# Kernel optimization log

Measured on AMD Instinct MI355X. Metric: run time of the kernel, lower is better.

The kernel has to match this reference:

```python
import jax, jax.numpy as jnp
import numpy as np

B_, P_, C_, S_ = 32, 16384, 2, 256   # batch, n_points, n_classes, box_size
LAT, ENC, H, NL = 10, 10, 64, 4       # latent dim, pos_enc_dim, hidden, n_layers


def setup_inputs() -> dict:
    key = jax.random.key(0)
    ks = jax.random.split(key, 10)
    z = jax.random.normal(ks[0], (B_, LAT), jnp.float32)
    orientation = jax.random.normal(ks[1], (B_, 3, 3), jnp.float32)  # rotation matrices
    shift = jax.random.normal(ks[2], (B_, 2), jnp.float32)           # pixel shifts
    # Gaussian center positions in box units [-0.37, 0.37] (stay inside box)
    model_positions = (jax.random.uniform(ks[3], (P_, 3), jnp.float32) - 0.5) * 0.74
    D_in = 6 * ENC + LAT
    W_in = jax.random.normal(ks[4], (D_in, H), jnp.float32) / jnp.sqrt(D_in * 1.0)
    W_layers = jax.random.normal(ks[5], (NL, H, H), jnp.float32) / jnp.sqrt(H * 1.0)
    W_out1 = jax.random.normal(ks[6], (H, 3), jnp.float32) / jnp.sqrt(H * 1.0)
    # original zero-fills this; use small values so the displacement path is nontrivial
    W_out2 = jax.random.normal(ks[7], (3, 3), jnp.float32) * 0.01
    amp = 30.0 * jnp.ones((C_, P_), jnp.float32)
    ampvar = 0.5 * jax.random.normal(ks[8], (C_, P_), jnp.float32)
    A = jnp.ones((C_,), jnp.float32)                 # smoother amplitudes
    Bp = jnp.linspace(0.01, 0.05, C_, dtype=jnp.float32)  # smoother widths
    return dict(z=z, orientation=orientation, shift=shift,
                model_positions=model_positions, W_in=W_in, W_layers=W_layers,
                W_out1=W_out1, W_out2=W_out2, amp=amp, ampvar=ampvar, A=A, Bp=Bp)


def positional_encoding(pos, enc_dim, box_size):
    # geometric frequency ladder from 1 to box_size/2, sin/cos per coordinate -> 6*enc_dim feats
    freqs = (box_size / 2.0) ** (jnp.arange(enc_dim, dtype=pos.dtype) / (enc_dim - 1))
    k = 2.0 * jnp.pi * pos[..., None] * freqs        # [..., 3, enc_dim]
    enc = jnp.concatenate([jnp.sin(k), jnp.cos(k)], axis=-1)
    return enc.reshape(pos.shape[:-1] + (6 * enc_dim,))


def mlp(x, W_in, W_layers, W1, W2):
    h = x @ W_in                                     # input layer, no activation
    for i in range(W_layers.shape[0]):
        h = jax.nn.elu(h @ W_layers[i])              # LinearBlock = Linear + ELU
    return jax.nn.elu(h @ W1) @ W2                   # output head


def points_to_images(pos2d, amps, S):
    # pos2d [B,P,2] in box units; amps [B,C,P]; bilinear splat -> [B,C,S,S]
    px = jnp.clip((pos2d + 0.5) * S, 0.0, S - 1.001)
    x0 = jnp.floor(px[..., 0]).astype(jnp.int32)
    y0 = jnp.floor(px[..., 1]).astype(jnp.int32)
    fx = px[..., 0] - x0
    fy = px[..., 1] - y0
    x1 = jnp.minimum(x0 + 1, S - 1)
    y1 = jnp.minimum(y0 + 1, S - 1)
    idx = jnp.stack([y0 * S + x0, y0 * S + x1, y1 * S + x0, y1 * S + x1], 0)      # [4,B,P]
    w = jnp.stack([(1 - fx) * (1 - fy), fx * (1 - fy), (1 - fx) * fy, fx * fy], 0)  # [4,B,P]

    def splat_one(idx_b, w_b, amp_b):
        # idx_b [4,P], w_b [4,P], amp_b [C,P]
        C = amp_b.shape[0]
        vals = amp_b[:, None, :] * w_b[None]          # [C,4,P]
        img = jnp.zeros((C, S * S), vals.dtype)
        img = img.at[:, idx_b.reshape(-1)].add(vals.reshape(C, -1))
        return img.reshape(C, S, S)

    return jax.vmap(splat_one, in_axes=(1, 1, 0))(idx, w, amps)


def fourier_smooth(ims, A, Bcoef):
    # ims [B,C,S,S] -> per-class Gaussian filter in Fourier space, sum over classes
    S = ims.shape[-1]
    c = (jnp.arange(S) - S // 2).astype(ims.dtype)
    R = jnp.sqrt(c[:, None] ** 2 + c[None, :] ** 2)   # centered radial grid
    FF = jnp.exp(-(Bcoef[:, None, None] ** 2) * R) * A[:, None, None] ** 2  # [C,S,S]
    FF = jnp.fft.ifftshift(FF, axes=(-2, -1))
    out = jnp.fft.ifft2(jnp.sum(FF[None] * jnp.fft.fft2(ims), axis=1))
    return jnp.real(out)                              # [B,S,S]


def fourier_shift_2d(ims, sx, sy):
    S = ims.shape[-1]
    f = jnp.fft.fftfreq(S).astype(ims.dtype)
    phase = jnp.exp(-2j * jnp.pi * (f[None, None, :] * sx[:, None, None]
                                    + f[None, :, None] * sy[:, None, None]))
    return jnp.real(jnp.fft.ifft2(jnp.fft.fft2(ims) * phase))


def reference(z, orientation, shift, model_positions, W_in, W_layers, W_out1, W_out2, amp, ampvar, A, Bp):
    B = z.shape[0]
    P = model_positions.shape[0]
    enc = positional_encoding(model_positions, ENC, S_)            # [P, 6*ENC]
    x = jnp.concatenate([
        jnp.broadcast_to(enc[None], (B, P, enc.shape[-1])),
        jnp.broadcast_to(z[:, None, :], (B, P, z.shape[-1]))], axis=-1)
    displacements = mlp(x, W_in, W_layers, W_out1, W_out2)         # [B,P,3]
    final_positions = model_positions[None] + displacements        # [B,P,3]
    projected = jnp.einsum('bij,bpj->bpi', orientation, final_positions)[..., :2]
    wamp = amp * jax.nn.softmax(ampvar, axis=0)                    # [C,P]
    wamp = jnp.broadcast_to(wamp[None], (B,) + wamp.shape)
    imgs = points_to_images(projected, wamp, S_)                   # [B,C,S,S]
    imgs = fourier_smooth(imgs, A, Bp)                             # [B,S,S]
    imgs = fourier_shift_2d(imgs, shift[:, 0], shift[:, 1])
    return imgs, final_positions, displacements
```

## Files before the change

### kernel.cpp

```cpp
#include <hip/hip_runtime.h>
#include <math.h>

static constexpr int Bn = 32, Pn = 16384, Cn = 2, Sn = 256;
static constexpr int KXD = 132;

#define TWO_PI_F 6.28318530717958647692f
#define SPLAT_SCALE 2048.0f
#define SPLAT_INV   (1.0f / 2048.0f)

typedef float v4f __attribute__((ext_vector_type(4)));
typedef short v8s __attribute__((ext_vector_type(8)));

__device__ __forceinline__ float elu_f(float x) {
  return x > 0.0f ? x : (__expf(x) - 1.0f);
}

__device__ __forceinline__ unsigned short f2bf(float x) {
  unsigned int u = __float_as_uint(x);
  u = u + 0x7FFFu + ((u >> 16) & 1u);
  return (unsigned short)(u >> 16);
}

__device__ __forceinline__ int cvt_pk_bf16(float lo, float hi) {
  int r;
  asm("v_cvt_pk_bf16_f32 %0, %1, %2" : "=v"(r) : "v"(lo), "v"(hi));
  return r;
}

__device__ __forceinline__ void fft256(float* re, float* im,
                                       const float* twr, const float* twi,
                                       int lane, bool inverse) {
  #pragma unroll
  for (int q = 0; q < 4; q++) {
    int t = lane + q * 64;
    int r = (int)(__brev((unsigned)t) >> 24);
    if (t < r) {
      float a = re[t]; re[t] = re[r]; re[r] = a;
      float b = im[t]; im[t] = im[r]; im[r] = b;
    }
  }
  __syncthreads();
  #pragma unroll
  for (int s = 1; s <= 8; s++) {
    int half = 1 << (s - 1);
    #pragma unroll
    for (int q = 0; q < 2; q++) {
      int bf = lane + q * 64;
      int j = bf & (half - 1);
      int grp = bf >> (s - 1);
      int i0 = (grp << s) + j;
      int i1 = i0 + half;
      int tx = j << (8 - s);
      float wr = twr[tx];
      float wi = twi[tx];
      if (inverse) wi = -wi;
      float xr = re[i1], xi = im[i1];
      float tr = fmaf(xr, wr, -xi * wi);
      float ti = fmaf(xr, wi,  xi * wr);
      float ar = re[i0], ai = im[i0];
      re[i0] = ar + tr; im[i0] = ai + ti;
      re[i1] = ar - tr; im[i1] = ai - ti;
    }
    __syncthreads();
  }
}

__global__ __launch_bounds__(64) void enc_kernel(const float* __restrict__ mp,
                                                 const float* __restrict__ W_in,
                                                 float* __restrict__ encpart) {
  __shared__ float ebuf[60][64];
  int tid = threadIdx.x;
  int p = blockIdx.x * 64 + tid;
  #pragma unroll
  for (int c = 0; c < 3; c++) {
    float pos = mp[p * 3 + c];
    #pragma unroll
    for (int i = 0; i < 10; i++) {
      float freq = powf(128.0f, (float)i / 9.0f);
      float ang = (TWO_PI_F * pos) * freq;
      ebuf[c * 20 + i][tid]      = sinf(ang);
      ebuf[c * 20 + 10 + i][tid] = cosf(ang);
    }
  }
  float h[64];
  #pragma unroll
  for (int j = 0; j < 64; j++) h[j] = 0.0f;
  for (int k = 0; k < 60; k++) {
    float ek = ebuf[k][tid];
    const float* wr = W_in + k * 64;
    #pragma unroll
    for (int j = 0; j < 64; j++) h[j] = fmaf(ek, wr[j], h[j]);
  }
  float* o = encpart + (size_t)p * 64;
  #pragma unroll
  for (int j = 0; j < 64; j++) o[j] = h[j];
}

__global__ __launch_bounds__(256) void prep_kernel(const float* __restrict__ z,
                                                   const float* __restrict__ W_in,
                                                   const float* __restrict__ W_layers,
                                                   float* __restrict__ zpart,
                                                   unsigned short* __restrict__ Wfrag) {
  int idx = blockIdx.x * 256 + threadIdx.x;
  if (idx < 2048) {
    int b = idx >> 6, j = idx & 63;
    float s = 0.0f;
    #pragma unroll
    for (int k = 0; k < 10; k++) s = fmaf(z[b * 10 + k], W_in[(60 + k) * 64 + j], s);
    zpart[b * 64 + j] = s;
  } else {
    int t2 = idx - 2048;
    int L = t2 >> 9, m = (t2 >> 7) & 3, s = (t2 >> 6) & 1, lane = t2 & 63;
    #pragma unroll
    for (int i = 0; i < 8; i++) {
      int k = s * 32 + ((lane >> 4) * 8) + i;
      int j = m * 16 + (lane & 15);
      Wfrag[(size_t)t2 * 8 + i] = f2bf(W_layers[L * 4096 + k * 64 + j]);
    }
  }
}

__device__ __forceinline__ void regroup(const v4f* acc, v8s* Bf,
                                        int srcA, int srcB, bool hi) {
  union U4 { int u[4]; v8s v; };
  int pk[4][2];
  #pragma unroll
  for (int m = 0; m < 4; m++) {
    pk[m][0] = cvt_pk_bf16(acc[m][0], acc[m][1]);
    pk[m][1] = cvt_pk_bf16(acc[m][2], acc[m][3]);
  }
  #pragma unroll
  for (int s = 0; s < 2; s++) {
    int t00 = __builtin_amdgcn_ds_bpermute(srcA, pk[2 * s][0]);
    int t01 = __builtin_amdgcn_ds_bpermute(srcA, pk[2 * s + 1][0]);
    int t10 = __builtin_amdgcn_ds_bpermute(srcA, pk[2 * s][1]);
    int t11 = __builtin_amdgcn_ds_bpermute(srcA, pk[2 * s + 1][1]);
    int t20 = __builtin_amdgcn_ds_bpermute(srcB, pk[2 * s][0]);
    int t21 = __builtin_amdgcn_ds_bpermute(srcB, pk[2 * s + 1][0]);
    int t30 = __builtin_amdgcn_ds_bpermute(srcB, pk[2 * s][1]);
    int t31 = __builtin_amdgcn_ds_bpermute(srcB, pk[2 * s + 1][1]);
    U4 u;
    u.u[0] = hi ? t01 : t00;
    u.u[1] = hi ? t11 : t10;
    u.u[2] = hi ? t21 : t20;
    u.u[3] = hi ? t31 : t30;
    Bf[s] = u.v;
  }
}

__global__ __launch_bounds__(256) void mlp_mfma32_kernel(
    const float* __restrict__ encpart, const float* __restrict__ zpart,
    const unsigned short* __restrict__ Wfrag,
    const float* __restrict__ W_out1, const float* __restrict__ W_out2,
    const float* __restrict__ mp, const float* __restrict__ orient,
    const float* __restrict__ amp, const float* __restrict__ ampvar,
    float4* __restrict__ rec, int* __restrict__ stripCntSeg,
    float* __restrict__ out_fp, float* __restrict__ out_disp) {
  __shared__ int h16[16];
  int tid = threadIdx.x;
  int lane = tid & 63;
  int wave = tid >> 6;
  int wid = blockIdx.x * 4 + wave;
  int b = __builtin_amdgcn_readfirstlane(wid >> 9);
  int pbase = (wid & 511) * 32;
  int g = lane >> 4;
  int p0 = pbase + (lane & 15);
  int p1 = p0 + 16;

  if (tid < 16) h16[tid] = 0;
  __syncthreads();

  union U4 { int u[4]; v8s v; };

  v8s Bf0[2], Bf1[2];
  #pragma unroll
  for (int s = 0; s < 2; s++) {
    int k0 = s * 32 + g * 8;
    const float4* z4 = (const float4*)(zpart + b * 64 + k0);
    float4 z0 = z4[0], z1 = z4[1];
    {
      const float4* e4 = (const float4*)(encpart + (size_t)p0 * 64 + k0);
      float4 e0 = e4[0], e1 = e4[1];
      U4 u;
      u.u[0] = cvt_pk_bf16(e0.x + z0.x, e0.y + z0.y);
      u.u[1] = cvt_pk_bf16(e0.z + z0.z, e0.w + z0.w);
      u.u[2] = cvt_pk_bf16(e1.x + z1.x, e1.y + z1.y);
      u.u[3] = cvt_pk_bf16(e1.z + z1.z, e1.w + z1.w);
      Bf0[s] = u.v;
    }
    {
      const float4* e4 = (const float4*)(encpart + (size_t)p1 * 64 + k0);
      float4 e0 = e4[0], e1 = e4[1];
      U4 u;
      u.u[0] = cvt_pk_bf16(e0.x + z0.x, e0.y + z0.y);
      u.u[1] = cvt_pk_bf16(e0.z + z0.z, e0.w + z0.w);
      u.u[2] = cvt_pk_bf16(e1.x + z1.x, e1.y + z1.y);
      u.u[3] = cvt_pk_bf16(e1.z + z1.z, e1.w + z1.w);
      Bf1[s] = u.v;
    }
  }

  int srcA = ((((lane >> 4) & 1) * 32) + (lane & 15)) << 2;
  int srcB = srcA + 64;
  bool hi = (lane >> 5) & 1;

  const v8s* WfragV = (const v8s*)Wfrag;
  v4f acc0[4], acc1[4];

  #pragma unroll 1
  for (int L = 0; L < 4; L++) {
    v8s Af[4][2];
    #pragma unroll
    for (int m = 0; m < 4; m++)
      #pragma unroll
      for (int s = 0; s < 2; s++)
        Af[m][s] = WfragV[(size_t)(((L * 4 + m) * 2 + s) * 64) + lane];

    #pragma unroll
    for (int m = 0; m < 4; m++) {
      acc0[m] = (v4f){0.f, 0.f, 0.f, 0.f};
      acc1[m] = (v4f){0.f, 0.f, 0.f, 0.f};
    }
    #pragma unroll
    for (int s = 0; s < 2; s++) {
      #pragma unroll
      for (int m = 0; m < 4; m++)
        acc0[m] = __builtin_amdgcn_mfma_f32_16x16x32_bf16(Af[m][s], Bf0[s], acc0[m], 0, 0, 0);
      #pragma unroll
      for (int m = 0; m < 4; m++)
        acc1[m] = __builtin_amdgcn_mfma_f32_16x16x32_bf16(Af[m][s], Bf1[s], acc1[m], 0, 0, 0);
    }

    #pragma unroll
    for (int m = 0; m < 4; m++)
      #pragma unroll
      for (int r = 0; r < 4; r++) {
        acc0[m][r] = elu_f(acc0[m][r]);
        acc1[m][r] = elu_f(acc1[m][r]);
      }

    if (L < 3) {
      regroup(acc0, Bf0, srcA, srcB, hi);
      regroup(acc1, Bf1, srcA, srcB, hi);
    }
  }

  float o00 = 0.f, o01 = 0.f, o02 = 0.f;
  float o10 = 0.f, o11 = 0.f, o12 = 0.f;
  #pragma unroll
  for (int m = 0; m < 4; m++) {
    int jb = m * 16 + g * 4;
    const float4* w4 = (const float4*)(W_out1 + jb * 3);
    float4 wa = w4[0], wb = w4[1], wc = w4[2];
    o00 += acc0[m][0] * wa.x + acc0[m][1] * wa.w + acc0[m][2] * wb.z + acc0[m][3] * wc.y;
    o01 += acc0[m][0] * wa.y + acc0[m][1] * wb.x + acc0[m][2] * wb.w + acc0[m][3] * wc.z;
    o02 += acc0[m][0] * wa.z + acc0[m][1] * wb.y + acc0[m][2] * wc.x + acc0[m][3] * wc.w;
    o10 += acc1[m][0] * wa.x + acc1[m][1] * wa.w + acc1[m][2] * wb.z + acc1[m][3] * wc.y;
    o11 += acc1[m][0] * wa.y + acc1[m][1] * wb.x + acc1[m][2] * wb.w + acc1[m][3] * wc.z;
    o12 += acc1[m][0] * wa.z + acc1[m][1] * wb.y + acc1[m][2] * wc.x + acc1[m][3] * wc.w;
  }
  o00 += __shfl_xor(o00, 16, 64); o00 += __shfl_xor(o00, 32, 64);
  o01 += __shfl_xor(o01, 16, 64); o01 += __shfl_xor(o01, 32, 64);
  o02 += __shfl_xor(o02, 16, 64); o02 += __shfl_xor(o02, 32, 64);
  o10 += __shfl_xor(o10, 16, 64); o10 += __shfl_xor(o10, 32, 64);
  o11 += __shfl_xor(o11, 16, 64); o11 += __shfl_xor(o11, 32, 64);
  o12 += __shfl_xor(o12, 16, 64); o12 += __shfl_xor(o12, 32, 64);

  o00 = elu_f(o00); o01 = elu_f(o01); o02 = elu_f(o02);
  o10 = elu_f(o10); o11 = elu_f(o11); o12 = elu_f(o12);

  float W0 = W_out2[0], W1 = W_out2[1], W2 = W_out2[2];
  float W3 = W_out2[3], W4 = W_out2[4], W5 = W_out2[5];
  float W6 = W_out2[6], W7 = W_out2[7], W8 = W_out2[8];

  float d00 = o00 * W0 + o01 * W3 + o02 * W6;
  float d01 = o00 * W1 + o01 * W4 + o02 * W7;
  float d02 = o00 * W2 + o01 * W5 + o02 * W8;
  float d10 = o10 * W0 + o11 * W3 + o12 * W6;
  float d11 = o10 * W1 + o11 * W4 + o12 * W7;
  float d12 = o10 * W2 + o11 * W5 + o12 * W8;

  float m00 = mp[p0 * 3 + 0], m01 = mp[p0 * 3 + 1], m02 = mp[p0 * 3 + 2];
  float m10 = mp[p1 * 3 + 0], m11 = mp[p1 * 3 + 1], m12 = mp[p1 * 3 + 2];
  float f00 = m00 + d00, f01 = m01 + d01, f02 = m02 + d02;
  float f10 = m10 + d10, f11 = m11 + d11, f12 = m12 + d12;

  size_t ob0 = ((size_t)b * Pn + p0) * 3;
  size_t ob1 = ((size_t)b * Pn + p1) * 3;
  if (g == 2) {
    out_disp[ob0 + 0] = d00; out_disp[ob0 + 1] = d01; out_disp[ob0 + 2] = d02;
    out_fp[ob0 + 0] = f00; out_fp[ob0 + 1] = f01; out_fp[ob0 + 2] = f02;
  }
  if (g == 3) {
    out_disp[ob1 + 0] = d10; out_disp[ob1 + 1] = d11; out_disp[ob1 + 2] = d12;
    out_fp[ob1 + 0] = f10; out_fp[ob1 + 1] = f11; out_fp[ob1 + 2] = f12;
  }

  const float* R = orient + b * 9;
  float px0 = R[0] * f00 + R[1] * f01 + R[2] * f02;
  float py0 = R[3] * f00 + R[4] * f01 + R[5] * f02;
  float px1 = R[0] * f10 + R[1] * f11 + R[2] * f12;
  float py1 = R[3] * f10 + R[4] * f11 + R[5] * f12;

  float a00 = ampvar[p0], a01 = ampvar[Pn + p0];
  float mx0 = fmaxf(a00, a01);
  float e00 = __expf(a00 - mx0), e01 = __expf(a01 - mx0);
  float inv0 = 1.0f / (e00 + e01);
  float w00a = amp[p0] * e00 * inv0;
  float w01a = amp[Pn + p0] * e01 * inv0;
  float a10 = ampvar[p1], a11 = ampvar[Pn + p1];
  float mx1 = fmaxf(a10, a11);
  float e10 = __expf(a10 - mx1), e11 = __expf(a11 - mx1);
  float inv1 = 1.0f / (e10 + e11);
  float w10a = amp[p1] * e10 * inv1;
  float w11a = amp[Pn + p1] * e11 * inv1;

  float pxp0 = fminf(fmaxf((px0 + 0.5f) * 256.0f, 0.0f), 254.999f);
  float pyp0 = fminf(fmaxf((py0 + 0.5f) * 256.0f, 0.0f), 254.999f);
  float pxp1 = fminf(fmaxf((px1 + 0.5f) * 256.0f, 0.0f), 254.999f);
  float pyp1 = fminf(fmaxf((py1 + 0.5f) * 256.0f, 0.0f), 254.999f);

  if (g == 0) {
    atomicAdd(&h16[((int)pyp0) >> 4], 1);
    rec[(size_t)b * Pn + p0] = make_float4(pxp0, pyp0, w00a, w01a);
  }
  if (g == 1) {
    atomicAdd(&h16[((int)pyp1) >> 4], 1);
    rec[(size_t)b * Pn + p1] = make_float4(pxp1, pyp1, w10a, w11a);
  }
  __syncthreads();
  int bblk = __builtin_amdgcn_readfirstlane(blockIdx.x >> 7);
  int seg  = __builtin_amdgcn_readfirstlane((blockIdx.x & 127) >> 4);
  if (tid < 16 && h16[tid] != 0)
    atomicAdd(&stripCntSeg[(bblk * 8 + seg) * 16 + tid], h16[tid]);
}

__global__ __launch_bounds__(256) void scatter16_kernel(const float4* __restrict__ rec,
                                                        const int* __restrict__ stripCntSeg,
                                                        float4* __restrict__ sorted) {
  __shared__ int tot[16], start[16], cur[16];
  int blk = blockIdx.x;
  int b = blk >> 3, seg = blk & 7;
  int tid = threadIdx.x;
  int myoff = 0;
  if (tid < 16) {
    int acc = 0, so = 0;
    #pragma unroll
    for (int s = 0; s < 8; s++) {
      int c = stripCntSeg[(b * 8 + s) * 16 + tid];
      if (s < seg) so += c;
      acc += c;
    }
    tot[tid] = acc; myoff = so;
  }
  __syncthreads();
  if (tid == 0) { int a = 0; for (int i = 0; i < 16; i++) { start[i] = a; a += tot[i]; } }
  __syncthreads();
  if (tid < 16) cur[tid] = start[tid] + myoff;
  __syncthreads();
  int base = seg * 2048;
  for (int i = base + tid; i < base + 2048; i += 256) {
    float4 r = rec[(size_t)b * Pn + i];
    int strip = ((int)r.y) >> 4;
    int slot = atomicAdd(&cur[strip], 1);
    sorted[(size_t)b * Pn + slot] = r;
  }
}

__global__ __launch_bounds__(256) void splat_fft_rows_T(const float4* __restrict__ sorted,
                                                        const int* __restrict__ stripCntSeg,
                                                        float2* __restrict__ ws1) {
  __shared__ float sre[16][257], sim[16][257];
  __shared__ float twr[128], twi[128];
  __shared__ int tot[16], start[16];
  int tid = threadIdx.x;
  int lane = tid & 63, wave = tid >> 6;
  int blk = blockIdx.x;
  int chunk = blk & 15, b = blk >> 4;
  for (int t = tid; t < 128; t += 256) {
    float ang = -TWO_PI_F * (float)t / 256.0f;
    twr[t] = cosf(ang); twi[t] = sinf(ang);
  }
  if (tid < 16) {
    int acc = 0;
    #pragma unroll
    for (int s = 0; s < 8; s++) acc += stripCntSeg[(b * 8 + s) * 16 + tid];
    tot[tid] = acc;
  }
  float* fre = &sre[0][0];
  float* fim = &sim[0][0];
  int* ire = (int*)fre;
  int* iim = (int*)fim;
  for (int j = tid; j < 16 * 257; j += 256) { ire[j] = 0; iim[j] = 0; }
  __syncthreads();
  if (tid == 0) { int a = 0; for (int i = 0; i < 16; i++) { start[i] = a; a += tot[i]; } }
  __syncthreads();

  int lo = (chunk > 0) ? start[chunk - 1] : start[0];
  int hi = start[chunk] + tot[chunk];
  int ybase = chunk * 16;
  const float4* rb = sorted + (size_t)b * Pn;
  for (int i = lo + tid; i < hi; i += 256) {
    float4 r = rb[i];
    int y0 = (int)r.y;
    int d = y0 - ybase;
    if (d >= -1 && d <= 15) {
      int x0 = (int)r.x;
      int x1 = x0 + 1;
      float fx = r.x - (float)x0, fy = r.y - (float)y0;
      float w00 = (1.f - fx) * (1.f - fy), w10 = fx * (1.f - fy);
      float w01 = (1.f - fx) * fy,         w11 = fx * fy;
      if (d >= 0) {
        int o = d * 257;
        atomicAdd(&ire[o + x0], __float2int_rn(r.z * w00 * SPLAT_SCALE));
        atomicAdd(&ire[o + x1], __float2int_rn(r.z * w10 * SPLAT_SCALE));
        atomicAdd(&iim[o + x0], __float2int_rn(r.w * w00 * SPLAT_SCALE));
        atomicAdd(&iim[o + x1], __float2int_rn(r.w * w10 * SPLAT_SCALE));
      }
      if (d <= 14) {
        int o = (d + 1) * 257;
        atomicAdd(&ire[o + x0], __float2int_rn(r.z * w01 * SPLAT_SCALE));
        atomicAdd(&ire[o + x1], __float2int_rn(r.z * w11 * SPLAT_SCALE));
        atomicAdd(&iim[o + x0], __float2int_rn(r.w * w01 * SPLAT_SCALE));
        atomicAdd(&iim[o + x1], __float2int_rn(r.w * w11 * SPLAT_SCALE));
      }
    }
  }
  __syncthreads();
  for (int j = tid; j < 16 * 257; j += 256) {
    fre[j] = (float)ire[j] * SPLAT_INV;
    fim[j] = (float)iim[j] * SPLAT_INV;
  }
  __syncthreads();

  #pragma unroll 1
  for (int rnd = 0; rnd < 4; rnd++) {
    int row = wave * 4 + rnd;
    fft256(&sre[row][0], &sim[row][0], twr, twi, lane, false);
  }
  #pragma unroll 1
  for (int ko = 0; ko < 9; ko++) {
    int kx = ko * 16 + (tid >> 4);
    int ysub = tid & 15;
    if (kx < KXD) {
      int m = (256 - kx) & 255;
      float zr = sre[ysub][kx], zi = sim[ysub][kx];
      float mr = sre[ysub][m],  mi = sim[ysub][m];
      float z0r = 0.5f * (zr + mr), z0i = 0.5f * (zi - mi);
      float z1r = 0.5f * (zi + mi), z1i = 0.5f * (mr - zr);
      size_t y = (size_t)(chunk * 16 + ysub);
      ws1[((size_t)(b * 2 + 0) * KXD + kx) * 256 + y] = make_float2(z0r, z0i);
      ws1[((size_t)(b * 2 + 1) * KXD + kx) * 256 + y] = make_float2(z1r, z1i);
    }
  }
}

__global__ __launch_bounds__(256) void fft_mid_T(const float2* __restrict__ ws1,
                                                 float2* __restrict__ A2,
                                                 const float* __restrict__ shift,
                                                 const float* __restrict__ Aarr,
                                                 const float* __restrict__ Bparr) {
  __shared__ float sre[4][257], sim[4][257];
  __shared__ float wre[4][257], wim[4][257];
  __shared__ float twr[128], twi[128];
  int tid = threadIdx.x;
  int lane = tid & 63, wave = tid >> 6;
  int blk = blockIdx.x;
  int b = blk / 33, c33 = blk % 33;
  int kx = c33 * 4 + wave;
  for (int t = tid; t < 128; t += 256) {
    float ang = -TWO_PI_F * (float)t / 256.0f;
    twr[t] = cosf(ang); twi[t] = sinf(ang);
  }
  __syncthreads();
  float A0 = Aarr[0], A1 = Aarr[1], B0 = Bparr[0], B1 = Bparr[1];
  float sy = shift[b * 2 + 1];
  const float2* r0 = ws1 + ((size_t)(b * 2 + 0) * KXD + kx) * 256;
  const float2* r1 = ws1 + ((size_t)(b * 2 + 1) * KXD + kx) * 256;
  #pragma unroll
  for (int q = 0; q < 4; q++) {
    int i = lane + q * 64;
    float2 v0 = r0[i], v1 = r1[i];
    sre[wave][i] = v0.x; sim[wave][i] = v0.y;
    wre[wave][i] = v1.x; wim[wave][i] = v1.y;
  }
  fft256(&sre[wave][0], &sim[wave][0], twr, twi, lane, false);
  fft256(&wre[wave][0], &wim[wave][0], twr, twi, lane, false);
  float rx = (kx <= 128) ? (float)kx : (float)(256 - kx);
  #pragma unroll
  for (int q = 0; q < 4; q++) {
    int ky = lane + q * 64;
    float ry = (ky <= 128) ? (float)ky : (float)(256 - ky);
    float R = sqrtf(rx * rx + ry * ry);
    float FF0 = A0 * A0 * __expf(-B0 * B0 * R);
    float FF1 = A1 * A1 * __expf(-B1 * B1 * R);
    float Gr = FF0 * sre[wave][ky] + FF1 * wre[wave][ky];
    float Gi = FF0 * sim[wave][ky] + FF1 * wim[wave][ky];
    float fk = (float)((ky < 128) ? ky : ky - 256) / 256.0f;
    float th = -TWO_PI_F * fk * sy;
    float cc = __cosf(th), ss = __sinf(th);
    sre[wave][ky] = Gr * cc - Gi * ss;
    sim[wave][ky] = Gr * ss + Gi * cc;
  }
  fft256(&sre[wave][0], &sim[wave][0], twr, twi, lane, true);
  const float inv = 1.0f / 256.0f;
  int kx0 = c33 * 4;
  #pragma unroll 1
  for (int yo = 0; yo < 4; yo++) {
    int ksub = tid & 3;
    int y = yo * 64 + (tid >> 2);
    int kxw = kx0 + ksub;
    float vr = sre[ksub][y] * inv, vi = sim[ksub][y] * inv;
    if (kxw <= 128)
      A2[(size_t)b * 65536 + (size_t)y * 256 + kxw] = make_float2(vr, vi);
    if (kxw >= 1 && kxw <= 127)
      A2[(size_t)b * 65536 + (size_t)y * 256 + (256 - kxw)] = make_float2(vr, -vi);
  }
}

__global__ __launch_bounds__(256) void fft_final_pk(const float2* __restrict__ A2t,
                                                    const float* __restrict__ shift,
                                                    float* __restrict__ out_imgs) {
  __shared__ float re[4][257], im[4][257];
  __shared__ float twr[128], twi[128];
  int tid = threadIdx.x;
  int lane = tid & 63, wave = tid >> 6;
  int blk = blockIdx.x;
  int b = blk >> 5, grp = blk & 31;
  int y0 = grp * 8 + wave * 2;
  int y1 = y0 + 1;
  for (int t = tid; t < 128; t += 256) {
    float ang = -TWO_PI_F * (float)t / 256.0f;
    twr[t] = cosf(ang); twi[t] = sinf(ang);
  }
  float sx = shift[b * 2 + 0];
  const float2* row0 = A2t + (size_t)b * 65536 + (size_t)y0 * 256;
  const float2* row1 = A2t + (size_t)b * 65536 + (size_t)y1 * 256;
  float g0r[4], g0i[4], g1r[4], g1i[4];
  #pragma unroll
  for (int q = 0; q < 4; q++) {
    int k = lane + q * 64;
    float2 v0 = row0[k], v1 = row1[k];
    float fk = (float)((k < 128) ? k : k - 256) / 256.0f;
    float th = -TWO_PI_F * fk * sx;
    float c = __cosf(th), s = __sinf(th);
    g0r[q] = v0.x * c - v0.y * s;  g0i[q] = v0.x * s + v0.y * c;
    g1r[q] = v1.x * c - v1.y * s;  g1i[q] = v1.x * s + v1.y * c;
  }
  int src = (64 - lane) & 63;
  float s0r[4], s0i[4], s1r[4], s1i[4];
  #pragma unroll
  for (int j = 0; j < 4; j++) {
    s0r[j] = __shfl(g0r[j], src, 64);  s0i[j] = __shfl(g0i[j], src, 64);
    s1r[j] = __shfl(g1r[j], src, 64);  s1i[j] = __shfl(g1i[j], src, 64);
  }
  bool l0 = (lane == 0);
  #pragma unroll
  for (int q = 0; q < 4; q++) {
    const int qa = 3 - q;
    const int qb = (4 - q) & 3;
    float m0r = l0 ? s0r[qb] : s0r[qa];
    float m0i = l0 ? s0i[qb] : s0i[qa];
    float m1r = l0 ? s1r[qb] : s1r[qa];
    float m1i = l0 ? s1i[qb] : s1i[qa];
    float h0r = 0.5f * (g0r[q] + m0r), h0i = 0.5f * (g0i[q] - m0i);
    float h1r = 0.5f * (g1r[q] + m1r), h1i = 0.5f * (g1i[q] - m1i);
    int k = lane + q * 64;
    re[wave][k] = h0r - h1i;
    im[wave][k] = h0i + h1r;
  }
  fft256(&re[wave][0], &im[wave][0], twr, twi, lane, true);
  const float inv = 1.0f / 256.0f;
  float* o0 = out_imgs + (size_t)b * 65536 + (size_t)y0 * 256;
  float* o1 = out_imgs + (size_t)b * 65536 + (size_t)y1 * 256;
  #pragma unroll
  for (int q = 0; q < 4; q++) {
    int x = lane + q * 64;
    o0[x] = re[wave][x] * inv;
    o1[x] = im[wave][x] * inv;
  }
}

extern "C" void kernel_launch(void* const* d_in, const int* in_sizes, int n_in,
                              void* d_out, int out_size, void* d_ws, size_t ws_size,
                              hipStream_t stream) {
  (void)in_sizes; (void)n_in; (void)out_size; (void)ws_size;
  const float* z       = (const float*)d_in[0];
  const float* orient  = (const float*)d_in[1];
  const float* shift   = (const float*)d_in[2];
  const float* mp      = (const float*)d_in[3];
  const float* W_in    = (const float*)d_in[4];
  const float* W_layers= (const float*)d_in[5];
  const float* W_out1  = (const float*)d_in[6];
  const float* W_out2  = (const float*)d_in[7];
  const float* amp     = (const float*)d_in[8];
  const float* ampvar  = (const float*)d_in[9];
  const float* Aarr    = (const float*)d_in[10];
  const float* Bparr   = (const float*)d_in[11];

  char* ws0 = (char*)d_ws;
  float*  encpart = (float*)ws0;
  float2* A2      = (float2*)ws0;
  char* wsB = ws0 + 19922944;
  float2* ws1     = (float2*)wsB;
  float4* rec     = (float4*)(wsB + 17301504);
  float4* sorted  = (float4*)(wsB + 25690112);
  float*  zpart   = (float*)(wsB + 34078720);
  unsigned short* Wfrag = (unsigned short*)(wsB + 34078720 + 8192);
  int* stripCntSeg = (int*)(wsB + 34078720 + 40960);

  float* out      = (float*)d_out;
  float* out_imgs = out;
  float* out_fp   = out + (size_t)Bn * Sn * Sn;
  float* out_disp = out_fp + (size_t)Bn * Pn * 3;

  hipMemsetAsync(stripCntSeg, 0, Bn * 8 * 16 * sizeof(int), stream);
  enc_kernel<<<Pn / 64, 64, 0, stream>>>(mp, W_in, encpart);
  prep_kernel<<<16, 256, 0, stream>>>(z, W_in, W_layers, zpart, Wfrag);
  mlp_mfma32_kernel<<<(Bn * Pn / 32) / 4, 256, 0, stream>>>(
      encpart, zpart, Wfrag, W_out1, W_out2, mp, orient, amp, ampvar,
      rec, stripCntSeg, out_fp, out_disp);
  scatter16_kernel<<<Bn * 8, 256, 0, stream>>>(rec, stripCntSeg, sorted);
  splat_fft_rows_T<<<Bn * 16, 256, 0, stream>>>(sorted, stripCntSeg, ws1);
  fft_mid_T<<<Bn * 33, 256, 0, stream>>>(ws1, A2, shift, Aarr, Bparr);
  fft_final_pk<<<Bn * 32, 256, 0, stream>>>(A2, shift, out_imgs);
}
```

Before: 187.2 us.

## Process 64 points per wave in MLP kernel and fold counter memset into prep

Each wave now handles four 16-point column tiles instead of two. The per-layer weight fragments are reused across twice as many MFMAs, and every lane does useful epilogue work instead of only a quarter of them. The separate memset launch is replaced by zeroing the strip counters inside prep_kernel, which drops one stream operation. The cost is a doubled accumulator and B-fragment register footprint, which may lower occupancy, and half as many blocks in the grid.

```diff
diff --git a/kernel.cpp b/kernel.cpp
--- a/kernel.cpp
+++ b/kernel.cpp
@@ -100,8 +100,10 @@
                                                    const float* __restrict__ W_in,
                                                    const float* __restrict__ W_layers,
                                                    float* __restrict__ zpart,
-                                                   unsigned short* __restrict__ Wfrag) {
+                                                   unsigned short* __restrict__ Wfrag,
+                                                   int* __restrict__ stripCntSeg) {
   int idx = blockIdx.x * 256 + threadIdx.x;
+  stripCntSeg[idx] = 0;
   if (idx < 2048) {
     int b = idx >> 6, j = idx & 63;
     float s = 0.0f;
@@ -148,7 +150,7 @@
   }
 }
 
-__global__ __launch_bounds__(256) void mlp_mfma32_kernel(
+__global__ __launch_bounds__(256) void mlp_mfma64_kernel(
     const float* __restrict__ encpart, const float* __restrict__ zpart,
     const unsigned short* __restrict__ Wfrag,
     const float* __restrict__ W_out1, const float* __restrict__ W_out2,
@@ -161,51 +163,42 @@
   int lane = tid & 63;
   int wave = tid >> 6;
   int wid = blockIdx.x * 4 + wave;
-  int b = __builtin_amdgcn_readfirstlane(wid >> 9);
-  int pbase = (wid & 511) * 32;
+  int b = __builtin_amdgcn_readfirstlane(wid >> 8);
+  int pbase = (wid & 255) * 64;
   int g = lane >> 4;
-  int p0 = pbase + (lane & 15);
-  int p1 = p0 + 16;
+  int l15 = lane & 15;
 
   if (tid < 16) h16[tid] = 0;
   __syncthreads();
 
   union U4 { int u[4]; v8s v; };
 
-  v8s Bf0[2], Bf1[2];
+  v8s Bf[4][2];
   #pragma unroll
   for (int s = 0; s < 2; s++) {
     int k0 = s * 32 + g * 8;
     const float4* z4 = (const float4*)(zpart + b * 64 + k0);
     float4 z0 = z4[0], z1 = z4[1];
-    {
-      const float4* e4 = (const float4*)(encpart + (size_t)p0 * 64 + k0);
+    #pragma unroll
+    for (int k2 = 0; k2 < 4; k2++) {
+      int pk = pbase + k2 * 16 + l15;
+      const float4* e4 = (const float4*)(encpart + (size_t)pk * 64 + k0);
       float4 e0 = e4[0], e1 = e4[1];
       U4 u;
       u.u[0] = cvt_pk_bf16(e0.x + z0.x, e0.y + z0.y);
       u.u[1] = cvt_pk_bf16(e0.z + z0.z, e0.w + z0.w);
       u.u[2] = cvt_pk_bf16(e1.x + z1.x, e1.y + z1.y);
       u.u[3] = cvt_pk_bf16(e1.z + z1.z, e1.w + z1.w);
-      Bf0[s] = u.v;
-    }
-    {
-      const float4* e4 = (const float4*)(encpart + (size_t)p1 * 64 + k0);
-      float4 e0 = e4[0], e1 = e4[1];
-      U4 u;
-      u.u[0] = cvt_pk_bf16(e0.x + z0.x, e0.y + z0.y);
-      u.u[1] = cvt_pk_bf16(e0.z + z0.z, e0.w + z0.w);
-      u.u[2] = cvt_pk_bf16(e1.x + z1.x, e1.y + z1.y);
-      u.u[3] = cvt_pk_bf16(e1.z + z1.z, e1.w + z1.w);
-      Bf1[s] = u.v;
-    }
-  }
-
-  int srcA = ((((lane >> 4) & 1) * 32) + (lane & 15)) << 2;
+      Bf[k2][s] = u.v;
+    }
+  }
+
+  int srcA = ((((lane >> 4) & 1) * 32) + l15) << 2;
   int srcB = srcA + 64;
   bool hi = (lane >> 5) & 1;
 
   const v8s* WfragV = (const v8s*)Wfrag;
-  v4f acc0[4], acc1[4];
+  v4f acc[4][4];
 
   #pragma unroll 1
   for (int L = 0; L < 4; L++) {
@@ -217,120 +210,93 @@
         Af[m][s] = WfragV[(size_t)(((L * 4 + m) * 2 + s) * 64) + lane];
 
     #pragma unroll
-    for (int m = 0; m < 4; m++) {
-      acc0[m] = (v4f){0.f, 0.f, 0.f, 0.f};
-      acc1[m] = (v4f){0.f, 0.f, 0.f, 0.f};
-    }
-    #pragma unroll
-    for (int s = 0; s < 2; s++) {
+    for (int k2 = 0; k2 < 4; k2++)
       #pragma unroll
       for (int m = 0; m < 4; m++)
-        acc0[m] = __builtin_amdgcn_mfma_f32_16x16x32_bf16(Af[m][s], Bf0[s], acc0[m], 0, 0, 0);
+        acc[k2][m] = (v4f){0.f, 0.f, 0.f, 0.f};
+    #pragma unroll
+    for (int s = 0; s < 2; s++)
+      #pragma unroll
+      for (int k2 = 0; k2 < 4; k2++)
+        #pragma unroll
+        for (int m = 0; m < 4; m++)
+          acc[k2][m] = __builtin_amdgcn_mfma_f32_16x16x32_bf16(Af[m][s], Bf[k2][s], acc[k2][m], 0, 0, 0);
+
+    #pragma unroll
+    for (int k2 = 0; k2 < 4; k2++)
       #pragma unroll
       for (int m = 0; m < 4; m++)
-        acc1[m] = __builtin_amdgcn_mfma_f32_16x16x32_bf16(Af[m][s], Bf1[s], acc1[m], 0, 0, 0);
-    }
-
-    #pragma unroll
-    for (int m = 0; m < 4; m++)
+        #pragma unroll
+        for (int r = 0; r < 4; r++)
+          acc[k2][m][r] = elu_f(acc[k2][m][r]);
+
+    if (L < 3) {
       #pragma unroll
-      for (int r = 0; r < 4; r++) {
-        acc0[m][r] = elu_f(acc0[m][r]);
-        acc1[m][r] = elu_f(acc1[m][r]);
-      }
-
-    if (L < 3) {
-      regroup(acc0, Bf0, srcA, srcB, hi);
-      regroup(acc1, Bf1, srcA, srcB, hi);
-    }
-  }
-
-  float o00 = 0.f, o01 = 0.f, o02 = 0.f;
-  float o10 = 0.f, o11 = 0.f, o12 = 0.f;
+      for (int k2 = 0; k2 < 4; k2++)
+        regroup(acc[k2], Bf[k2], srcA, srcB, hi);
+    }
+  }
+
+  float o[4][3];
+  #pragma unroll
+  for (int k2 = 0; k2 < 4; k2++) { o[k2][0] = 0.f; o[k2][1] = 0.f; o[k2][2] = 0.f; }
   #pragma unroll
   for (int m = 0; m < 4; m++) {
     int jb = m * 16 + g * 4;
     const float4* w4 = (const float4*)(W_out1 + jb * 3);
     float4 wa = w4[0], wb = w4[1], wc = w4[2];
-    o00 += acc0[m][0] * wa.x + acc0[m][1] * wa.w + acc0[m][2] * wb.z + acc0[m][3] * wc.y;
-    o01 += acc0[m][0] * wa.y + acc0[m][1] * wb.x + acc0[m][2] * wb.w + acc0[m][3] * wc.z;
-    o02 += acc0[m][0] * wa.z + acc0[m][1] * wb.y + acc0[m][2] * wc.x + acc0[m][3] * wc.w;
-    o10 += acc1[m][0] * wa.x + acc1[m][1] * wa.w + acc1[m][2] * wb.z + acc1[m][3] * wc.y;
-    o11 += acc1[m][0] * wa.y + acc1[m][1] * wb.x + acc1[m][2] * wb.w + acc1[m][3] * wc.z;
-    o12 += acc1[m][0] * wa.z + acc1[m][1] * wb.y + acc1[m][2] * wc.x + acc1[m][3] * wc.w;
-  }
-  o00 += __shfl_xor(o00, 16, 64); o00 += __shfl_xor(o00, 32, 64);
-  o01 += __shfl_xor(o01, 16, 64); o01 += __shfl_xor(o01, 32, 64);
-  o02 += __shfl_xor(o02, 16, 64); o02 += __shfl_xor(o02, 32, 64);
-  o10 += __shfl_xor(o10, 16, 64); o10 += __shfl_xor(o10, 32, 64);
-  o11 += __shfl_xor(o11, 16, 64); o11 += __shfl_xor(o11, 32, 64);
-  o12 += __shfl_xor(o12, 16, 64); o12 += __shfl_xor(o12, 32, 64);
-
-  o00 = elu_f(o00); o01 = elu_f(o01); o02 = elu_f(o02);
-  o10 = elu_f(o10); o11 = elu_f(o11); o12 = elu_f(o12);
-
-  float W0 = W_out2[0], W1 = W_out2[1], W2 = W_out2[2];
-  float W3 = W_out2[3], W4 = W_out2[4], W5 = W_out2[5];
-  float W6 = W_out2[6], W7 = W_out2[7], W8 = W_out2[8];
-
-  float d00 = o00 * W0 + o01 * W3 + o02 * W6;
-  float d01 = o00 * W1 + o01 * W4 + o02 * W7;
-  float d02 = o00 * W2 + o01 * W5 + o02 * W8;
-  float d10 = o10 * W0 + o11 * W3 + o12 * W6;
-  float d11 = o10 * W1 + o11 * W4 + o12 * W7;
-  float d12 = o10 * W2 + o11 * W5 + o12 * W8;
-
-  float m00 = mp[p0 * 3 + 0], m01 = mp[p0 * 3 + 1], m02 = mp[p0 * 3 + 2];
-  float m10 = mp[p1 * 3 + 0], m11 = mp[p1 * 3 + 1], m12 = mp[p1 * 3 + 2];
-  float f00 = m00 + d00, f01 = m01 + d01, f02 = m02 + d02;
-  float f10 = m10 + d10, f11 = m11 + d11, f12 = m12 + d12;
-
-  size_t ob0 = ((size_t)b * Pn + p0) * 3;
-  size_t ob1 = ((size_t)b * Pn + p1) * 3;
-  if (g == 2) {
-    out_disp[ob0 + 0] = d00; out_disp[ob0 + 1] = d01; out_disp[ob0 + 2] = d02;
-    out_fp[ob0 + 0] = f00; out_fp[ob0 + 1] = f01; out_fp[ob0 + 2] = f02;
-  }
-  if (g == 3) {
-    out_disp[ob1 + 0] = d10; out_disp[ob1 + 1] = d11; out_disp[ob1 + 2] = d12;
-    out_fp[ob1 + 0] = f10; out_fp[ob1 + 1] = f11; out_fp[ob1 + 2] = f12;
-  }
+    #pragma unroll
+    for (int k2 = 0; k2 < 4; k2++) {
+      o[k2][0] += acc[k2][m][0] * wa.x + acc[k2][m][1] * wa.w + acc[k2][m][2] * wb.z + acc[k2][m][3] * wc.y;
+      o[k2][1] += acc[k2][m][0] * wa.y + acc[k2][m][1] * wb.x + acc[k2][m][2] * wb.w + acc[k2][m][3] * wc.z;
+      o[k2][2] += acc[k2][m][0] * wa.z + acc[k2][m][1] * wb.y + acc[k2][m][2] * wc.x + acc[k2][m][3] * wc.w;
+    }
+  }
+  #pragma unroll
+  for (int k2 = 0; k2 < 4; k2++)
+    #pragma unroll
+    for (int c = 0; c < 3; c++) {
+      o[k2][c] += __shfl_xor(o[k2][c], 16, 64);
+      o[k2][c] += __shfl_xor(o[k2][c], 32, 64);
+    }
+
+  float s0 = (g == 0) ? o[0][0] : (g == 1) ? o[1][0] : (g == 2) ? o[2][0] : o[3][0];
+  float s1 = (g == 0) ? o[0][1] : (g == 1) ? o[1][1] : (g == 2) ? o[2][1] : o[3][1];
+  float s2 = (g == 0) ? o[0][2] : (g == 1) ? o[1][2] : (g == 2) ? o[2][2] : o[3][2];
+  s0 = elu_f(s0); s1 = elu_f(s1); s2 = elu_f(s2);
+
+  float d0 = s0 * W_out2[0] + s1 * W_out2[3] + s2 * W_out2[6];
+  float d1 = s0 * W_out2[1] + s1 * W_out2[4] + s2 * W_out2[7];
+  float d2 = s0 * W_out2[2] + s1 * W_out2[5] + s2 * W_out2[8];
+
+  int pg = pbase + g * 16 + l15;
+  float m0 = mp[pg * 3 + 0], m1 = mp[pg * 3 + 1], m2 = mp[pg * 3 + 2];
+  float f0 = m0 + d0, f1 = m1 + d1, f2 = m2 + d2;
+
+  size_t ob = ((size_t)b * Pn + pg) * 3;
+  out_disp[ob + 0] = d0; out_disp[ob + 1] = d1; out_disp[ob + 2] = d2;
+  out_fp[ob + 0] = f0; out_fp[ob + 1] = f1; out_fp[ob + 2] = f2;
 
   const float* R = orient + b * 9;
-  float px0 = R[0] * f00 + R[1] * f01 + R[2] * f02;
-  float py0 = R[3] * f00 + R[4] * f01 + R[5] * f02;
-  float px1 = R[0] * f10 + R[1] * f11 + R[2] * f12;
-  float py1 = R[3] * f10 + R[4] * f11 + R[5] * f12;
-
-  float a00 = ampvar[p0], a01 = ampvar[Pn + p0];
-  float mx0 = fmaxf(a00, a01);
-  float e00 = __expf(a00 - mx0), e01 = __expf(a01 - mx0);
-  float inv0 = 1.0f / (e00 + e01);
-  float w00a = amp[p0] * e00 * inv0;
-  float w01a = amp[Pn + p0] * e01 * inv0;
-  float a10 = ampvar[p1], a11 = ampvar[Pn + p1];
-  float mx1 = fmaxf(a10, a11);
-  float e10 = __expf(a10 - mx1), e11 = __expf(a11 - mx1);
-  float inv1 = 1.0f / (e10 + e11);
-  float w10a = amp[p1] * e10 * inv1;
-  float w11a = amp[Pn + p1] * e11 * inv1;
-
-  float pxp0 = fminf(fmaxf((px0 + 0.5f) * 256.0f, 0.0f), 254.999f);
-  float pyp0 = fminf(fmaxf((py0 + 0.5f) * 256.0f, 0.0f), 254.999f);
-  float pxp1 = fminf(fmaxf((px1 + 0.5f) * 256.0f, 0.0f), 254.999f);
-  float pyp1 = fminf(fmaxf((py1 + 0.5f) * 256.0f, 0.0f), 254.999f);
-
-  if (g == 0) {
-    atomicAdd(&h16[((int)pyp0) >> 4], 1);
-    rec[(size_t)b * Pn + p0] = make_float4(pxp0, pyp0, w00a, w01a);
-  }
-  if (g == 1) {
-    atomicAdd(&h16[((int)pyp1) >> 4], 1);
-    rec[(size_t)b * Pn + p1] = make_float4(pxp1, pyp1, w10a, w11a);
-  }
-  __syncthreads();
-  int bblk = __builtin_amdgcn_readfirstlane(blockIdx.x >> 7);
-  int seg  = __builtin_amdgcn_readfirstlane((blockIdx.x & 127) >> 4);
+  float px = R[0] * f0 + R[1] * f1 + R[2] * f2;
+  float py = R[3] * f0 + R[4] * f1 + R[5] * f2;
+
+  float a0 = ampvar[pg], a1 = ampvar[Pn + pg];
+  float mx = fmaxf(a0, a1);
+  float e0 = __expf(a0 - mx), e1 = __expf(a1 - mx);
+  float inv = 1.0f / (e0 + e1);
+  float w0 = amp[pg] * e0 * inv;
+  float w1 = amp[Pn + pg] * e1 * inv;
+
+  float pxp = fminf(fmaxf((px + 0.5f) * 256.0f, 0.0f), 254.999f);
+  float pyp = fminf(fmaxf((py + 0.5f) * 256.0f, 0.0f), 254.999f);
+
+  atomicAdd(&h16[((int)pyp) >> 4], 1);
+  rec[(size_t)b * Pn + pg] = make_float4(pxp, pyp, w0, w1);
+
+  __syncthreads();
+  int bblk = __builtin_amdgcn_readfirstlane(blockIdx.x >> 6);
+  int seg  = __builtin_amdgcn_readfirstlane((blockIdx.x >> 3) & 7);
   if (tid < 16 && h16[tid] != 0)
     atomicAdd(&stripCntSeg[(bblk * 8 + seg) * 16 + tid], h16[tid]);
 }
@@ -614,10 +580,9 @@
   float* out_fp   = out + (size_t)Bn * Sn * Sn;
   float* out_disp = out_fp + (size_t)Bn * Pn * 3;
 
-  hipMemsetAsync(stripCntSeg, 0, Bn * 8 * 16 * sizeof(int), stream);
   enc_kernel<<<Pn / 64, 64, 0, stream>>>(mp, W_in, encpart);
-  prep_kernel<<<16, 256, 0, stream>>>(z, W_in, W_layers, zpart, Wfrag);
-  mlp_mfma32_kernel<<<(Bn * Pn / 32) / 4, 256, 0, stream>>>(
+  prep_kernel<<<16, 256, 0, stream>>>(z, W_in, W_layers, zpart, Wfrag, stripCntSeg);
+  mlp_mfma64_kernel<<<(Bn * Pn / 64) / 4, 256, 0, stream>>>(
       encpart, zpart, Wfrag, W_out1, W_out2, mp, orient, amp, ampvar,
       rec, stripCntSeg, out_fp, out_disp);
   scatter16_kernel<<<Bn * 8, 256, 0, stream>>>(rec, stripCntSeg, sorted);
```

Measured after the change: 186.1 us. Within noise of the previous version (-0.6%).
